# Performance work log

Hardware: AMD Instinct MI355X
Metric: run time of the kernel (lower is better)

## Reference

```python
import jax, jax.numpy as jnp
import numpy as np

N_HOST = 20000   # Host nodes
N_FLOW = 200000  # NetworkFlow nodes
E_HF = 400000    # edges per communicates direction
E_REL = 800000   # NetworkFlow-related-NetworkFlow edges
G = 64           # graphs in batch
H = 128          # hidden_dim
FI = 97          # NetworkFlow input feature dim (hardcoded in source)
NC = 10          # num_classes
L = 3            # layers
VOCAB = 4000     # host embedding table size (hardcoded in source)


def setup_inputs() -> dict:
    key = jax.random.key(0)
    ks = iter(jax.random.split(key, 40))
    def n(shape, scale=1.0):
        return jax.random.normal(next(ks), shape, jnp.float32) * scale
    s = 0.02
    inp = {}
    inp['host_node_ids'] = jax.random.randint(next(ks), (N_HOST,), 0, VOCAB)
    inp['flow_x'] = n((N_FLOW, FI))
    inp['h2f_src'] = jax.random.randint(next(ks), (E_HF,), 0, N_HOST)
    inp['h2f_dst'] = jax.random.randint(next(ks), (E_HF,), 0, N_FLOW)
    inp['f2h_src'] = jax.random.randint(next(ks), (E_HF,), 0, N_FLOW)
    inp['f2h_dst'] = jax.random.randint(next(ks), (E_HF,), 0, N_HOST)
    inp['rel_src'] = jax.random.randint(next(ks), (E_REL,), 0, N_FLOW)
    inp['rel_dst'] = jax.random.randint(next(ks), (E_REL,), 0, N_FLOW)
    inp['flow_batch'] = jnp.sort(jax.random.randint(next(ks), (N_FLOW,), 0, G))
    # parameters
    inp['host_embed'] = n((VOCAB, H), s)
    # layer 0 (heterogeneous input dims): GraphConv = lin_rel(agg) + lin_root(x_dst)
    inp['Wr0_h2f'] = n((H, H), s);  inp['br0_h2f'] = jnp.zeros((H,), jnp.float32); inp['Wo0_h2f'] = n((FI, H), s)
    inp['Wr0_f2h'] = n((FI, H), s); inp['br0_f2h'] = jnp.zeros((H,), jnp.float32); inp['Wo0_f2h'] = n((H, H), s)
    inp['Wr0_rel'] = n((FI, H), s); inp['br0_rel'] = jnp.zeros((H,), jnp.float32); inp['Wo0_rel'] = n((FI, H), s)
    # layers 1..L-1 stacked: axis1 order = [h2f, f2h, rel]
    inp['Wr'] = n((L - 1, 3, H, H), s)
    inp['br'] = jnp.zeros((L - 1, 3, H), jnp.float32)
    inp['Wo'] = n((L - 1, 3, H, H), s)
    # classifier (second Linear corrected to hidden//2 -> hidden so shapes chain)
    inp['Wc1'] = n((H, H // 2), s); inp['bc1'] = jnp.zeros((H // 2,), jnp.float32)
    inp['Wc2'] = n((H // 2, H), s); inp['bc2'] = jnp.zeros((H,), jnp.float32)
    inp['Wc3'] = n((H, NC), s);     inp['bc3'] = jnp.zeros((NC,), jnp.float32)
    return inp


def _graphconv(x_src, x_dst, src, dst, n_dst, Wr, br, Wo):
    # PyG GraphConv: lin_rel(sum_{j in N(i)} x_j) + lin_root(x_i); lin_root has no bias
    agg = jax.ops.segment_sum(x_src[src], dst, num_segments=n_dst)  # [n_dst, d_src]
    return agg @ Wr + br + x_dst @ Wo


def reference(host_node_ids, flow_x, h2f_src, h2f_dst, f2h_src, f2h_dst, rel_src, rel_dst,
              flow_batch, host_embed,
              Wr0_h2f, br0_h2f, Wo0_h2f, Wr0_f2h, br0_f2h, Wo0_f2h, Wr0_rel, br0_rel, Wo0_rel,
              Wr, br, Wo, Wc1, bc1, Wc2, bc2, Wc3, bc3):
    x_host = host_embed[host_node_ids]  # [N_HOST, H]
    x_flow = flow_x                     # [N_FLOW, FI]
    # layer 0: HeteroConv aggr='sum' over edge types writing to same dst type
    nf = _graphconv(x_host, x_flow, h2f_src, h2f_dst, N_FLOW, Wr0_h2f, br0_h2f, Wo0_h2f) \
       + _graphconv(x_flow, x_flow, rel_src, rel_dst, N_FLOW, Wr0_rel, br0_rel, Wo0_rel)
    nh = _graphconv(x_flow, x_host, f2h_src, f2h_dst, N_HOST, Wr0_f2h, br0_f2h, Wo0_f2h)
    x_flow, x_host = jax.nn.relu(nf), jax.nn.relu(nh)  # dropout p=0.0 -> identity
    # layers 1..L-1 (relu after all but the last conv)
    for l in range(L - 1):
        nf = _graphconv(x_host, x_flow, h2f_src, h2f_dst, N_FLOW, Wr[l, 0], br[l, 0], Wo[l, 0]) \
           + _graphconv(x_flow, x_flow, rel_src, rel_dst, N_FLOW, Wr[l, 2], br[l, 2], Wo[l, 2])
        nh = _graphconv(x_flow, x_host, f2h_src, f2h_dst, N_HOST, Wr[l, 1], br[l, 1], Wo[l, 1])
        if l < L - 2:
            nf, nh = jax.nn.relu(nf), jax.nn.relu(nh)
        x_flow, x_host = nf, nh
    pooled = jax.ops.segment_max(x_flow, flow_batch, num_segments=G)  # global_max_pool [G, H]
    h = jax.nn.relu(pooled @ Wc1 + bc1)
    h = jax.nn.relu(h @ Wc2 + bc2)
    return h @ Wc3 + bc3  # [G, NC]
```

## Files before the change

kernel.cpp:

```cpp
#include <hip/hip_runtime.h>
#include <hip/hip_bf16.h>

using bf16 = __hip_bfloat16;

#define N_HOSTN 20000
#define N_FLOWN 200000
#define E_HFN   400000
#define E_RELN  800000
#define E_CMBN  1200000
#define GG      64
#define HH      128
#define FIN     97
#define NCN     10

#define NB_REL_E 3125
#define NB_HF_E  1563
#define NB_CMB_N 782
#define NB_F2H_N 79
#define NCH_REL 391
#define NCH_HF  196
#define PLC_REL (NCH_REL*8)
#define PLC_H2F (PLC_REL + NCH_HF*8)
#define PLC_ALL (PLC_H2F + NCH_HF*8)

#define AGG_CAP    768
#define AGGF_DPW   24
#define AGGF_BLK   2084
#define AGGH_DPW   12
#define AGGH_BLK   417

static inline int cdiv(long long a, long long b){ return (int)((a + b - 1) / b); }

__device__ __forceinline__ float bf2f(unsigned short u){
    return __uint_as_float(((unsigned)u) << 16);
}
__device__ __forceinline__ unsigned short f2bf(float f){
    unsigned u = __float_as_uint(f);
    unsigned r = u + 0x7FFFu + ((u >> 16) & 1u);
    return (unsigned short)(r >> 16);
}
__device__ __forceinline__ float loadf(const void* p, size_t i, int isbf){
    return isbf ? bf2f(((const unsigned short*)p)[i]) : ((const float*)p)[i];
}
__device__ __forceinline__ void acc8(float* a, uint4 z){
    a[0] += __uint_as_float(z.x << 16);
    a[1] += __uint_as_float(z.x & 0xFFFF0000u);
    a[2] += __uint_as_float(z.y << 16);
    a[3] += __uint_as_float(z.y & 0xFFFF0000u);
    a[4] += __uint_as_float(z.z << 16);
    a[5] += __uint_as_float(z.z & 0xFFFF0000u);
    a[6] += __uint_as_float(z.w << 16);
    a[7] += __uint_as_float(z.w & 0xFFFF0000u);
}

__global__ void k_detect(const unsigned short* x, int* flag){
    __shared__ int bad;
    if (threadIdx.x == 0) bad = 0;
    __syncthreads();
    int b = 0;
    for (int i = threadIdx.x; i < 4096; i += 256) {
        unsigned e = (x[i] >> 7) & 0xFFu;
        if (e >= 0x90u) b++;
    }
    if (b) atomicAdd(&bad, b);
    __syncthreads();
    if (threadIdx.x == 0) *flag = (bad == 0) ? 1 : 0;
}

__global__ void k_zero(float* p, size_t n){
    size_t i = (size_t)blockIdx.x * 256 + threadIdx.x;
    if (i < n) p[i] = 0.f;
}
__global__ void k_flag_us(unsigned short* out, int n, unsigned short val){
    int i = blockIdx.x * 256 + threadIdx.x;
    if (i < n) out[i] = val;
}
__global__ void k_gather_embed(const int* ids, const void* emb, float* out, const int* flagp){
    int i = blockIdx.x * 256 + threadIdx.x;
    if (i >= N_HOSTN * HH) return;
    int isbf = *flagp;
    int node = i >> 7, f = i & 127;
    out[i] = loadf(emb, (size_t)ids[node] * HH + f, isbf);
}
__global__ void k_pad_cast(const void* x, unsigned short* o, const int* flagp){
    int i = blockIdx.x * 256 + threadIdx.x;
    if (i >= N_FLOWN * 16) return;
    int isbf = *flagp;
    int row = i >> 4, c0 = (i & 15) * 8;
    unsigned short v[8];
    #pragma unroll
    for (int j = 0; j < 8; ++j) {
        int c = c0 + j;
        v[j] = (c < FIN) ? f2bf(loadf(x, (size_t)row * FIN + c, isbf)) : (unsigned short)0;
    }
    uint4 ov;
    ov.x = (unsigned)v[0] | ((unsigned)v[1] << 16);
    ov.y = (unsigned)v[2] | ((unsigned)v[3] << 16);
    ov.z = (unsigned)v[4] | ((unsigned)v[5] << 16);
    ov.w = (unsigned)v[6] | ((unsigned)v[7] << 16);
    *(uint4*)(o + (size_t)row * 128 + c0) = ov;
}

__global__ __launch_bounds__(256) void k_wprep_all(
    const void* Wr0_h2f, const void* br0_h2f, const void* Wo0_h2f,
    const void* Wr0_f2h, const void* br0_f2h, const void* Wo0_f2h,
    const void* Wr0_rel, const void* br0_rel, const void* Wo0_rel,
    const void* Wr_all, const void* br_all, const void* Wo_all,
    unsigned short* WBT0, unsigned short* WBT1, unsigned short* WBT2,
    float* w_h2f0, float* w_h2f1, float* w_h2f2,
    float* w_f2h0, float* w_f2h1, float* w_of2h0, float* w_of2h1,
    float* b_comb0, float* b_comb1, float* b_comb2, float* b_f2h0, float* b_f2h1,
    const int* flagp)
{
    const int bb = blockIdx.x, t = threadIdx.x;
    const int isbf = *flagp;
    if (bb < 384) {
        int layer = bb >> 7;
        int i = ((bb & 127) << 8) + t;
        int nn = i >> 7, k = i & 127;
        float v = 0.f;
        if (layer == 0) {
            if (k < FIN) {
                if (nn < 128) v = loadf(Wo0_h2f, (size_t)k*128+nn, isbf) + loadf(Wo0_rel, (size_t)k*128+nn, isbf);
                else          v = loadf(Wr0_rel, (size_t)k*128+(nn-128), isbf);
            }
        } else {
            size_t oW = (size_t)((layer - 1) * 3) * 16384;
            if (nn < 128) v = loadf(Wo_all, oW + (size_t)k*128+nn, isbf)
                            + loadf(Wo_all, oW + 2*16384 + (size_t)k*128+nn, isbf);
            else          v = loadf(Wr_all, oW + 2*16384 + (size_t)k*128+(nn-128), isbf);
        }
        unsigned short* W = (layer == 0) ? WBT0 : ((layer == 1) ? WBT1 : WBT2);
        W[(size_t)nn*128 + k] = f2bf(v);
    } else if (bb < 576) {
        int r = bb - 384; int layer = r >> 6; int i = ((r & 63) << 8) + t;
        float v;
        if (layer == 0) v = loadf(Wr0_h2f, (size_t)i, isbf);
        else            v = loadf(Wr_all, (size_t)((layer-1)*3)*16384 + i, isbf);
        ((layer == 0) ? w_h2f0 : ((layer == 1) ? w_h2f1 : w_h2f2))[i] = v;
    } else if (bb < 640) {
        int i = ((bb - 576) << 8) + t;
        int k = i >> 7;
        w_f2h0[i] = (k < FIN) ? loadf(Wr0_f2h, (size_t)i, isbf) : 0.f;
    } else if (bb < 704) {
        int i = ((bb - 640) << 8) + t;
        w_f2h1[i] = loadf(Wr_all, (size_t)1*16384 + i, isbf);
    } else if (bb < 768) {
        int i = ((bb - 704) << 8) + t;
        w_of2h0[i] = loadf(Wo0_f2h, (size_t)i, isbf);
    } else if (bb < 832) {
        int i = ((bb - 768) << 8) + t;
        w_of2h1[i] = loadf(Wo_all, (size_t)1*16384 + i, isbf);
    } else {
        if (t < 128) {
            b_comb0[t] = loadf(br0_h2f, t, isbf) + loadf(br0_rel, t, isbf);
            b_comb1[t] = loadf(br_all, 0*128 + t, isbf) + loadf(br_all, 2*128 + t, isbf);
            b_comb2[t] = loadf(br_all, 3*128 + t, isbf) + loadf(br_all, 5*128 + t, isbf);
            b_f2h0[t]  = loadf(br0_f2h, t, isbf);
            b_f2h1[t]  = loadf(br_all, 1*128 + t, isbf);
        }
    }
}

__global__ void k_zero2(int* c0, int* c1){
    int bb = blockIdx.x, t = threadIdx.x;
    if (bb < NB_CMB_N) { int i = bb * 256 + t; if (i < N_FLOWN) c0[i] = 0; }
    else               { int i = (bb - NB_CMB_N) * 256 + t; if (i < N_HOSTN) c1[i] = 0; }
}
__global__ void k_hist3(const int* drel, const int* dh2f, const int* df2h,
                        int* c_cmb, int* c_f2h){
    int bb = blockIdx.x, t = threadIdx.x;
    const int* dst; int* cnt; int E; int base;
    if (bb < NB_REL_E)                   { dst = drel; cnt = c_cmb; E = E_RELN; base = bb; }
    else if (bb < NB_REL_E + NB_HF_E)    { dst = dh2f; cnt = c_cmb; E = E_HFN;  base = bb - NB_REL_E; }
    else                                 { dst = df2h; cnt = c_f2h; E = E_HFN;  base = bb - NB_REL_E - NB_HF_E; }
    int e = base * 256 + t;
    if (e < E) atomicAdd(&cnt[dst[e]], 1);
}
__global__ __launch_bounds__(256) void k_scan1_2(
    const int* c0, int* rp0, int* bs0,
    const int* c1, int* rp1, int* bs1)
{
    __shared__ int s[256];
    int bb = blockIdx.x, t = threadIdx.x;
    const int* cnt; int* rp; int* bsum; int n; int base;
    if (bb < NB_CMB_N) { cnt = c0; rp = rp0; bsum = bs0; n = N_FLOWN; base = bb; }
    else               { cnt = c1; rp = rp1; bsum = bs1; n = N_HOSTN; base = bb - NB_CMB_N; }
    int i = base * 256 + t;
    int v = (i < n) ? cnt[i] : 0;
    s[t] = v; __syncthreads();
    for (int off = 1; off < 256; off <<= 1) {
        int x = (t >= off) ? s[t - off] : 0;
        __syncthreads();
        s[t] += x;
        __syncthreads();
    }
    if (i < n) rp[i] = s[t] - v;
    if (t == 255) bsum[base] = s[255];
}
__global__ __launch_bounds__(256) void k_scan2_2(int* bs0, int* bs1){
    __shared__ int s[256];
    __shared__ int carry;
    int t = threadIdx.x;
    int* bsum; int nb;
    if (blockIdx.x == 0) { bsum = bs0; nb = NB_CMB_N; }
    else                 { bsum = bs1; nb = NB_F2H_N; }
    if (t == 0) carry = 0;
    __syncthreads();
    for (int base = 0; base < nb; base += 256) {
        int i = base + t;
        int v = (i < nb) ? bsum[i] : 0;
        s[t] = v; __syncthreads();
        for (int off = 1; off < 256; off <<= 1) {
            int x = (t >= off) ? s[t - off] : 0;
            __syncthreads();
            s[t] += x;
            __syncthreads();
        }
        int excl = s[t] - v + carry;
        if (i < nb) bsum[i] = excl;
        __syncthreads();
        if (t == 255) carry += s[255];
        __syncthreads();
    }
}
__global__ void k_scan3_2(int* rp0, const int* bs0, int* w0,
                          int* rp1, const int* bs1, int* w1)
{
    int bb = blockIdx.x, t = threadIdx.x;
    int* rp; const int* bsum; int* wr; int n, E, base;
    if (bb < NB_CMB_N) { rp = rp0; bsum = bs0; wr = w0; n = N_FLOWN; E = E_CMBN; base = bb; }
    else               { rp = rp1; bsum = bs1; wr = w1; n = N_HOSTN; E = E_HFN;  base = bb - NB_CMB_N; }
    int i = base * 256 + t;
    if (i < n) { int v = rp[i] + bsum[base]; rp[i] = v; wr[i] = v; }
    if (i == 0) rp[n] = E;
}
__global__ __launch_bounds__(256) void k_place3c(
    const int* s0, const int* d0,
    const int* s1, const int* d1,
    const int* s2, const int* d2,
    int* w_cmb, int* e_cmb, int* w_f2h, int* e_f2h)
{
    const int bb = blockIdx.x;
    const int *src, *dst; int *wr, *ei; int E, divc, rb, soff;
    if (bb < PLC_REL)      { src=s0; dst=d0; wr=w_cmb; ei=e_cmb; E=E_RELN; divc=25000; rb=bb;          soff=0; }
    else if (bb < PLC_H2F) { src=s1; dst=d1; wr=w_cmb; ei=e_cmb; E=E_HFN;  divc=25000; rb=bb-PLC_REL;  soff=N_FLOWN; }
    else                   { src=s2; dst=d2; wr=w_f2h; ei=e_f2h; E=E_HFN;  divc=2500;  rb=bb-PLC_H2F;  soff=0; }
    const int cls  = rb & 7;
    const int base = (rb >> 3) * 2048;
    const int t = threadIdx.x;
    #pragma unroll
    for (int i = 0; i < 8; ++i) {
        const int e = base + t + i * 256;
        if (e < E) {
            const int d = dst[e];
            if (d / divc == cls) {
                const int pos = atomicAdd(&wr[d], 1);
                ei[pos] = src[e] + soff;
            }
        }
    }
}

__global__ __launch_bounds__(256) void k_gemm128(
    const void* X, int xmode, const float* W, const float* bias,
    void* Y, int ybf, int M, int K, int accum, int dorelu, const int* flagp)
{
    const int isbf = (xmode == 2) ? *flagp : xmode;
    const int tid  = threadIdx.x;
    const int row0 = blockIdx.x * 16;
    __shared__ float sX[16][132];
    if (!isbf && (K & 3) == 0) {
        const int kq = K >> 2;
        for (int i = tid; i < 16 * kq; i += 256) {
            int r = i / kq, c4 = (i - r * kq) * 4;
            int gr = row0 + r;
            float4 v = {0.f, 0.f, 0.f, 0.f};
            if (gr < M) v = *(const float4*)((const float*)X + (size_t)gr * K + c4);
            *(float4*)&sX[r][c4] = v;
        }
    } else {
        const int total = 16 * K;
        for (int i = tid; i < total; i += 256) {
            int r = i / K, c = i - r * K;
            int gr = row0 + r;
            sX[r][c] = (gr < M) ? loadf(X, (size_t)gr * K + c, isbf) : 0.f;
        }
    }
    __syncthreads();

    const int c4 = (tid & 31) * 4;
    const int rb = tid >> 5;
    float a0x=0,a0y=0,a0z=0,a0w=0, a1x=0,a1y=0,a1z=0,a1w=0;
    #pragma unroll 4
    for (int k = 0; k < K; ++k) {
        const float4 w = *(const float4*)(W + (size_t)k * 128 + c4);
        const float x0 = sX[rb][k];
        const float x1 = sX[rb + 8][k];
        a0x = fmaf(x0, w.x, a0x); a0y = fmaf(x0, w.y, a0y);
        a0z = fmaf(x0, w.z, a0z); a0w = fmaf(x0, w.w, a0w);
        a1x = fmaf(x1, w.x, a1x); a1y = fmaf(x1, w.y, a1y);
        a1z = fmaf(x1, w.z, a1z); a1w = fmaf(x1, w.w, a1w);
    }
    float bx=0, by=0, bz=0, bw=0;
    if (bias) { const float4 b = *(const float4*)(bias + c4); bx=b.x; by=b.y; bz=b.z; bw=b.w; }

    #pragma unroll
    for (int h = 0; h < 2; ++h) {
        const int rr = row0 + rb + (h ? 8 : 0);
        if (rr >= M) continue;
        float v0 = (h?a1x:a0x)+bx, v1 = (h?a1y:a0y)+by;
        float v2 = (h?a1z:a0z)+bz, v3 = (h?a1w:a0w)+bw;
        if (ybf) {
            unsigned short* p = (unsigned short*)Y + (size_t)rr * 128 + c4;
            ushort4 o; o.x=f2bf(v0); o.y=f2bf(v1); o.z=f2bf(v2); o.w=f2bf(v3);
            *(ushort4*)p = o;
        } else {
            float* p = (float*)Y + (size_t)rr * 128 + c4;
            if (accum) { v0+=p[0]; v1+=p[1]; v2+=p[2]; v3+=p[3]; }
            if (dorelu) { v0=fmaxf(v0,0.f); v1=fmaxf(v1,0.f); v2=fmaxf(v2,0.f); v3=fmaxf(v3,0.f); }
            float4 o; o.x=v0; o.y=v1; o.z=v2; o.w=v3;
            *(float4*)p = o;
        }
    }
}

__global__ __launch_bounds__(256) void k_gemm2in(
    const float* __restrict__ X1, const float* __restrict__ X2,
    const float* __restrict__ W1, const float* __restrict__ W2,
    const float* __restrict__ bias, float* __restrict__ Y, int M)
{
    const int tid  = threadIdx.x;
    const int row0 = blockIdx.x * 16;
    __shared__ float sX1[16][132];
    __shared__ float sX2[16][132];
    for (int i = tid; i < 16 * 32; i += 256) {
        int r = i >> 5, c4 = (i & 31) * 4;
        int gr = row0 + r;
        float4 v1 = {0.f, 0.f, 0.f, 0.f}, v2 = {0.f, 0.f, 0.f, 0.f};
        if (gr < M) {
            v1 = *(const float4*)(X1 + (size_t)gr * 128 + c4);
            v2 = *(const float4*)(X2 + (size_t)gr * 128 + c4);
        }
        *(float4*)&sX1[r][c4] = v1;
        *(float4*)&sX2[r][c4] = v2;
    }
    __syncthreads();

    const int c4 = (tid & 31) * 4;
    const int rb = tid >> 5;
    float a0x=0,a0y=0,a0z=0,a0w=0, a1x=0,a1y=0,a1z=0,a1w=0;
    #pragma unroll 4
    for (int k = 0; k < 128; ++k) {
        const float4 w = *(const float4*)(W1 + (size_t)k * 128 + c4);
        const float x0 = sX1[rb][k];
        const float x1 = sX1[rb + 8][k];
        a0x = fmaf(x0, w.x, a0x); a0y = fmaf(x0, w.y, a0y);
        a0z = fmaf(x0, w.z, a0z); a0w = fmaf(x0, w.w, a0w);
        a1x = fmaf(x1, w.x, a1x); a1y = fmaf(x1, w.y, a1y);
        a1z = fmaf(x1, w.z, a1z); a1w = fmaf(x1, w.w, a1w);
    }
    #pragma unroll 4
    for (int k = 0; k < 128; ++k) {
        const float4 w = *(const float4*)(W2 + (size_t)k * 128 + c4);
        const float x0 = sX2[rb][k];
        const float x1 = sX2[rb + 8][k];
        a0x = fmaf(x0, w.x, a0x); a0y = fmaf(x0, w.y, a0y);
        a0z = fmaf(x0, w.z, a0z); a0w = fmaf(x0, w.w, a0w);
        a1x = fmaf(x1, w.x, a1x); a1y = fmaf(x1, w.y, a1y);
        a1z = fmaf(x1, w.z, a1z); a1w = fmaf(x1, w.w, a1w);
    }
    const float4 b = *(const float4*)(bias + c4);
    #pragma unroll
    for (int h = 0; h < 2; ++h) {
        const int rr = row0 + rb + (h ? 8 : 0);
        if (rr >= M) continue;
        float4 o;
        o.x = fmaxf((h?a1x:a0x) + b.x, 0.f);
        o.y = fmaxf((h?a1y:a0y) + b.y, 0.f);
        o.z = fmaxf((h?a1z:a0z) + b.z, 0.f);
        o.w = fmaxf((h?a1w:a0w) + b.w, 0.f);
        *(float4*)(Y + (size_t)rr * 128 + c4) = o;
    }
}

typedef __attribute__((ext_vector_type(8))) short bfrag;
typedef __attribute__((ext_vector_type(4))) float f32x4;

#define GEMM_CHUNKS 4
#define GEMM_MROWS  (32 * GEMM_CHUNKS)

__global__ __launch_bounds__(512, 4) void k_gemm_mfma(
    const unsigned short* __restrict__ Abf, const unsigned short* __restrict__ WBT,
    unsigned short* __restrict__ Y1, unsigned short* __restrict__ Y2, int M)
{
    __shared__ unsigned short sA[32 * 128];
    __shared__ unsigned short sO[2][32][136];

    const int tid  = threadIdx.x;
    const int wave = tid >> 6;
    const int lane = tid & 63;
    const int quad = lane >> 4;
    const int l16  = lane & 15;
    const int nbase = wave * 32;

    bfrag breg[4][2];
    #pragma unroll
    for (int c = 0; c < 4; ++c)
        #pragma unroll
        for (int j = 0; j < 2; ++j)
            breg[c][j] = *(const bfrag*)(WBT + (size_t)(nbase + j * 16 + l16) * 128
                                              + c * 32 + quad * 8);

// ... 198 lines not shown
            const int s2 = (e + 2 < Wcap) ? sIdx[wave][e + 2 - W0] : ei[e + 2];
            const int s3 = (e + 3 < Wcap) ? sIdx[wave][e + 3 - W0] : ei[e + 3];
            const uint4 z0 = *(const uint4*)(Z + (size_t)s0 * 128 + f8);
            const uint4 z1 = *(const uint4*)(Z + (size_t)s1 * 128 + f8);
            const uint4 z2 = *(const uint4*)(Z + (size_t)s2 * 128 + f8);
            const uint4 z3 = *(const uint4*)(Z + (size_t)s3 * 128 + f8);
            acc8(a, z0); acc8(a, z1); acc8(a, z2); acc8(a, z3);
            e += 4; n -= 4;
        }
        if (n & 2) {
            const int s0 = (e     < Wcap) ? sIdx[wave][e     - W0] : ei[e];
            const int s1 = (e + 1 < Wcap) ? sIdx[wave][e + 1 - W0] : ei[e + 1];
            const uint4 z0 = *(const uint4*)(Z + (size_t)s0 * 128 + f8);
            const uint4 z1 = *(const uint4*)(Z + (size_t)s1 * 128 + f8);
            acc8(a, z0); acc8(a, z1);
            e += 2;
        }
        if (n & 1) {
            const int s0 = (e < Wcap) ? sIdx[wave][e - W0] : ei[e];
            const uint4 z0 = *(const uint4*)(Z + (size_t)s0 * 128 + f8);
            acc8(a, z0);
        }

        if (act) {
            float4 oa, ob;
            oa.x = a[0]; oa.y = a[1]; oa.z = a[2]; oa.w = a[3];
            ob.x = a[4]; ob.y = a[5]; ob.z = a[6]; ob.w = a[7];
            *(float4*)(out + (size_t)d * 128 + f8)     = oa;
            *(float4*)(out + (size_t)d * 128 + f8 + 4) = ob;
        }
    }
}

#define PCHUNK 128
__global__ __launch_bounds__(128) void k_pool2(const unsigned short* xf, const int* batch,
                                               unsigned* bits){
    const int t = threadIdx.x;
    const int i0 = blockIdx.x * PCHUNK;
    const int iend = min(i0 + PCHUNK, N_FLOWN);
    if (i0 >= N_FLOWN) return;
    float cur = -3.4e38f;
    int curg = batch[i0];
    for (int i = i0; i < iend; ++i) {
        int g = batch[i];
        if (g != curg) {
            unsigned u = __float_as_uint(cur);
            unsigned ord = (u & 0x80000000u) ? ~u : (u | 0x80000000u);
            atomicMax(&bits[(size_t)curg * 128 + t], ord);
            cur = -3.4e38f; curg = g;
        }
        cur = fmaxf(cur, bf2f(xf[(size_t)i * 128 + t]));
    }
    unsigned u = __float_as_uint(cur);
    unsigned ord = (u & 0x80000000u) ? ~u : (u | 0x80000000u);
    atomicMax(&bits[(size_t)curg * 128 + t], ord);
}

__global__ __launch_bounds__(128) void k_classifier(
    const unsigned* bits,
    const void* Wc1, const void* bc1, const void* Wc2, const void* bc2,
    const void* Wc3, const void* bc3, void* out, const int* flagp)
{
    const int g = blockIdx.x, t = threadIdx.x;
    const int isbf = *flagp;
    __shared__ float sp[128], sh1[64], sh2[128];
    {
        unsigned ord = bits[(size_t)g * HH + t];
        unsigned u = (ord & 0x80000000u) ? (ord & 0x7FFFFFFFu) : ~ord;
        sp[t] = __uint_as_float(u);
    }
    __syncthreads();
    if (t < 64) {
        float a = loadf(bc1, t, isbf);
        #pragma unroll 4
        for (int k = 0; k < 128; ++k) a = fmaf(sp[k], loadf(Wc1, k * 64 + t, isbf), a);
        sh1[t] = fmaxf(a, 0.f);
    }
    __syncthreads();
    {
        float a = loadf(bc2, t, isbf);
        #pragma unroll 4
        for (int k = 0; k < 64; ++k) a = fmaf(sh1[k], loadf(Wc2, k * 128 + t, isbf), a);
        sh2[t] = fmaxf(a, 0.f);
    }
    __syncthreads();
    if (t < NCN) {
        float a = loadf(bc3, t, isbf);
        #pragma unroll 4
        for (int k = 0; k < 128; ++k) a = fmaf(sh2[k], loadf(Wc3, k * NCN + t, isbf), a);
        if (isbf) ((unsigned short*)out)[(size_t)g * NCN + t] = f2bf(a);
        else      ((float*)out)[(size_t)g * NCN + t] = a;
    }
}

extern "C" void kernel_launch(void* const* d_in, const int* in_sizes, int n_in,
                              void* d_out, int out_size, void* d_ws, size_t ws_size,
                              hipStream_t stream)
{
    const int*  host_ids   = (const int*) d_in[0];
    const void* flow_x     = d_in[1];
    const int*  h2f_src    = (const int*) d_in[2];
    const int*  h2f_dst    = (const int*) d_in[3];
    const int*  f2h_src    = (const int*) d_in[4];
    const int*  f2h_dst    = (const int*) d_in[5];
    const int*  rel_src    = (const int*) d_in[6];
    const int*  rel_dst    = (const int*) d_in[7];
    const int*  flow_batch = (const int*) d_in[8];
    const void* host_embed = d_in[9];
    const void* Wr0_h2f = d_in[10]; const void* br0_h2f = d_in[11]; const void* Wo0_h2f = d_in[12];
    const void* Wr0_f2h = d_in[13]; const void* br0_f2h = d_in[14]; const void* Wo0_f2h = d_in[15];
    const void* Wr0_rel = d_in[16]; const void* br0_rel = d_in[17]; const void* Wo0_rel = d_in[18];
    const void* Wr_all  = d_in[19];
    const void* br_all  = d_in[20];
    const void* Wo_all  = d_in[21];
    const void* Wc1 = d_in[22]; const void* bc1 = d_in[23];
    const void* Wc2 = d_in[24]; const void* bc2 = d_in[25];
    const void* Wc3 = d_in[26]; const void* bc3 = d_in[27];

    size_t off = 0;
    auto alloc = [&](size_t bytes) -> char* {
        char* p = (char*)d_ws + off;
        off += (bytes + 255) & ~(size_t)255;
        return p;
    };
    unsigned short* F1bf  = (unsigned short*)alloc((size_t)N_FLOWN * HH * 2);
    unsigned short* Froot = (unsigned short*)alloc((size_t)N_FLOWN * HH * 2);
    unsigned short* ZALL  = (unsigned short*)alloc((size_t)(N_FLOWN + N_HOSTN) * HH * 2);
    unsigned short* F2bf  = ZALL;
    unsigned short* HCbf  = ZALL + (size_t)N_FLOWN * HH;
    float* HA = (float*)alloc((size_t)N_HOSTN * HH * 4);
    float* HB = (float*)alloc((size_t)N_HOSTN * HH * 4);
    float* HD = (float*)alloc((size_t)N_HOSTN * HH * 4);
    unsigned short* WBT0 = (unsigned short*)alloc(256 * 128 * 2);
    unsigned short* WBT1 = (unsigned short*)alloc(256 * 128 * 2);
    unsigned short* WBT2 = (unsigned short*)alloc(256 * 128 * 2);
    float* w_h2f0  = (float*)alloc(128 * 128 * 4);
    float* w_h2f1  = (float*)alloc(128 * 128 * 4);
    float* w_h2f2  = (float*)alloc(128 * 128 * 4);
    float* w_f2h0  = (float*)alloc(128 * 128 * 4);
    float* w_f2h1  = (float*)alloc(128 * 128 * 4);
    float* w_of2h0 = (float*)alloc(128 * 128 * 4);
    float* w_of2h1 = (float*)alloc(128 * 128 * 4);
    float* b_comb0 = (float*)alloc(128 * 4);
    float* b_comb1 = (float*)alloc(128 * 4);
    float* b_comb2 = (float*)alloc(128 * 4);
    float* b_f2h0  = (float*)alloc(128 * 4);
    float* b_f2h1  = (float*)alloc(128 * 4);
    unsigned* poolbits = (unsigned*)alloc(GG * HH * 4);
    int* flagp = (int*)alloc(256);
    int* rp_cmb = (int*)alloc((N_FLOWN + 1) * 4);
    int* ei_cmb = (int*)alloc((size_t)E_CMBN * 4);
    int* rp_f2h = (int*)alloc((N_HOSTN + 1) * 4);
    int* ei_f2h = (int*)alloc((size_t)E_HFN * 4);
    int* wr_cmb = (int*)alloc((size_t)N_FLOWN * 4);
    int* wr_f2h = (int*)alloc((size_t)N_HOSTN * 4);
    int* bs0 = (int*)alloc(1024 * 4);
    int* bs2 = (int*)alloc(256 * 4);

    const int T = 256;
    #define GRID1(n) dim3(cdiv((long long)(n), T)), dim3(T), 0, stream

    if (off > ws_size) {
        k_flag_us<<<GRID1(out_size)>>>((unsigned short*)d_out, out_size, (unsigned short)0x4000);
        return;
    }

    k_detect<<<dim3(1), dim3(256), 0, stream>>>((const unsigned short*)flow_x, flagp);

    k_zero2 <<<dim3(NB_CMB_N + NB_F2H_N), dim3(256), 0, stream>>>(wr_cmb, wr_f2h);
    k_hist3 <<<dim3(NB_REL_E + 2*NB_HF_E), dim3(256), 0, stream>>>(rel_dst, h2f_dst, f2h_dst,
                                                                    wr_cmb, wr_f2h);
    k_scan1_2<<<dim3(NB_CMB_N + NB_F2H_N), dim3(256), 0, stream>>>(
        wr_cmb, rp_cmb, bs0, wr_f2h, rp_f2h, bs2);
    k_scan2_2<<<dim3(2), dim3(256), 0, stream>>>(bs0, bs2);
    k_scan3_2<<<dim3(NB_CMB_N + NB_F2H_N), dim3(256), 0, stream>>>(
        rp_cmb, bs0, wr_cmb, rp_f2h, bs2, wr_f2h);
    k_place3c<<<dim3(PLC_ALL), dim3(256), 0, stream>>>(
        rel_src, rel_dst, h2f_src, h2f_dst, f2h_src, f2h_dst,
        wr_cmb, ei_cmb, wr_f2h, ei_f2h);

    k_wprep_all<<<dim3(833), dim3(256), 0, stream>>>(
        Wr0_h2f, br0_h2f, Wo0_h2f, Wr0_f2h, br0_f2h, Wo0_f2h, Wr0_rel, br0_rel, Wo0_rel,
        Wr_all, br_all, Wo_all,
        WBT0, WBT1, WBT2, w_h2f0, w_h2f1, w_h2f2,
        w_f2h0, w_f2h1, w_of2h0, w_of2h1,
        b_comb0, b_comb1, b_comb2, b_f2h0, b_f2h1, flagp);

    k_gather_embed<<<GRID1(N_HOSTN * HH)>>>(host_ids, host_embed, HA, flagp);
    k_pad_cast<<<GRID1(N_FLOWN * 16)>>>(flow_x, F1bf, flagp);
    k_agg_host<<<dim3(AGGH_BLK), dim3(256), 0, stream>>>(F1bf, rp_f2h, ei_f2h, HD);
    k_gemm2in<<<dim3(cdiv(N_HOSTN,16)), dim3(256), 0, stream>>>(HD, HA, w_f2h0, w_of2h0, b_f2h0, HB, N_HOSTN);
    k_gemm128<<<dim3(cdiv(N_HOSTN,16)), dim3(256), 0, stream>>>(HA, 0, w_h2f0, nullptr, HCbf, 1, N_HOSTN, 128, 0, 0, flagp);
    k_gemm_mfma<<<dim3(cdiv(N_FLOWN, GEMM_MROWS)), dim3(512), 0, stream>>>(F1bf, WBT0, Froot, F2bf, N_FLOWN);
    k_agg_flow<<<dim3(AGGF_BLK), dim3(256), 0, stream>>>(ZALL, rp_cmb, ei_cmb,
                                                         Froot, b_comb0, F1bf, 1);

    k_agg_host<<<dim3(AGGH_BLK), dim3(256), 0, stream>>>(F1bf, rp_f2h, ei_f2h, HD);
    k_gemm128<<<dim3(cdiv(N_HOSTN,16)), dim3(256), 0, stream>>>(HB, 0, w_h2f1, nullptr, HCbf, 1, N_HOSTN, 128, 0, 0, flagp);
    k_gemm_mfma<<<dim3(cdiv(N_FLOWN, GEMM_MROWS)), dim3(512), 0, stream>>>(F1bf, WBT1, Froot, F2bf, N_FLOWN);
    k_agg_flow<<<dim3(AGGF_BLK), dim3(256), 0, stream>>>(ZALL, rp_cmb, ei_cmb,
                                                         Froot, b_comb1, F1bf, 1);
    k_gemm2in<<<dim3(cdiv(N_HOSTN,16)), dim3(256), 0, stream>>>(HD, HB, w_f2h1, w_of2h1, b_f2h1, HA, N_HOSTN);

    k_gemm128<<<dim3(cdiv(N_HOSTN,16)), dim3(256), 0, stream>>>(HA, 0, w_h2f2, nullptr, HCbf, 1, N_HOSTN, 128, 0, 0, flagp);
    k_gemm_mfma<<<dim3(cdiv(N_FLOWN, GEMM_MROWS)), dim3(512), 0, stream>>>(F1bf, WBT2, Froot, F2bf, N_FLOWN);
    k_agg_flow<<<dim3(AGGF_BLK), dim3(256), 0, stream>>>(ZALL, rp_cmb, ei_cmb,
                                                         Froot, b_comb2, F1bf, 0);

    k_zero<<<GRID1(GG * HH)>>>((float*)poolbits, (size_t)GG * HH);
    k_pool2<<<dim3(cdiv(N_FLOWN, PCHUNK)), dim3(128), 0, stream>>>(F1bf, flow_batch, poolbits);
    k_classifier<<<dim3(GG), dim3(128), 0, stream>>>(poolbits, Wc1, bc1, Wc2, bc2, Wc3, bc3,
                                                     d_out, flagp);
    #undef GRID1
}
```

Before: 941.4 us.

## Record per-edge ranks in histogram to make CSR placement atomic-free

The histogram kernel now stores the atomicAdd return value as each edge's rank within its destination bucket. The placement kernel then writes each edge directly to rowptr[dst] + rank, with no second round of atomics. This replaces the old 8-class partitioned scatter that re-read the edge arrays eight times. Rank and count scratch buffers reuse the HA/HB workspace, which assumes those buffers are free until they are written later. Ordering within a bucket becomes nondeterministic, but it already was.

```diff
diff --git a/kernel.cpp b/kernel.cpp
--- a/kernel.cpp
+++ b/kernel.cpp
@@ -17,11 +17,9 @@
 #define NB_HF_E  1563
 #define NB_CMB_N 782
 #define NB_F2H_N 79
-#define NCH_REL 391
-#define NCH_HF  196
-#define PLC_REL (NCH_REL*8)
-#define PLC_H2F (PLC_REL + NCH_HF*8)
-#define PLC_ALL (PLC_H2F + NCH_HF*8)
+#define PB_REL 782
+#define PB_HF  391
+#define PB_ALL (PB_REL + 2*PB_HF)
 
 #define AGG_CAP    768
 #define AGGF_DPW   24
@@ -168,14 +166,15 @@
     else               { int i = (bb - NB_CMB_N) * 256 + t; if (i < N_HOSTN) c1[i] = 0; }
 }
 __global__ void k_hist3(const int* drel, const int* dh2f, const int* df2h,
-                        int* c_cmb, int* c_f2h){
+                        int* c_cmb, int* c_f2h,
+                        int* rk_rel, int* rk_h2f, int* rk_f2h){
     int bb = blockIdx.x, t = threadIdx.x;
-    const int* dst; int* cnt; int E; int base;
-    if (bb < NB_REL_E)                   { dst = drel; cnt = c_cmb; E = E_RELN; base = bb; }
-    else if (bb < NB_REL_E + NB_HF_E)    { dst = dh2f; cnt = c_cmb; E = E_HFN;  base = bb - NB_REL_E; }
-    else                                 { dst = df2h; cnt = c_f2h; E = E_HFN;  base = bb - NB_REL_E - NB_HF_E; }
+    const int* dst; int* cnt; int* rk; int E; int base;
+    if (bb < NB_REL_E)                   { dst = drel; cnt = c_cmb; rk = rk_rel; E = E_RELN; base = bb; }
+    else if (bb < NB_REL_E + NB_HF_E)    { dst = dh2f; cnt = c_cmb; rk = rk_h2f; E = E_HFN;  base = bb - NB_REL_E; }
+    else                                 { dst = df2h; cnt = c_f2h; rk = rk_f2h; E = E_HFN;  base = bb - NB_REL_E - NB_HF_E; }
     int e = base * 256 + t;
-    if (e < E) atomicAdd(&cnt[dst[e]], 1);
+    if (e < E) rk[e] = atomicAdd(&cnt[dst[e]], 1);
 }
 __global__ __launch_bounds__(256) void k_scan1_2(
     const int* c0, int* rp0, int* bs0,
@@ -224,40 +223,36 @@
         __syncthreads();
     }
 }
-__global__ void k_scan3_2(int* rp0, const int* bs0, int* w0,
-                          int* rp1, const int* bs1, int* w1)
+__global__ void k_scan3_2(int* rp0, const int* bs0,
+                          int* rp1, const int* bs1)
 {
     int bb = blockIdx.x, t = threadIdx.x;
-    int* rp; const int* bsum; int* wr; int n, E, base;
-    if (bb < NB_CMB_N) { rp = rp0; bsum = bs0; wr = w0; n = N_FLOWN; E = E_CMBN; base = bb; }
-    else               { rp = rp1; bsum = bs1; wr = w1; n = N_HOSTN; E = E_HFN;  base = bb - NB_CMB_N; }
+    int* rp; const int* bsum; int n, E, base;
+    if (bb < NB_CMB_N) { rp = rp0; bsum = bs0; n = N_FLOWN; E = E_CMBN; base = bb; }
+    else               { rp = rp1; bsum = bs1; n = N_HOSTN; E = E_HFN;  base = bb - NB_CMB_N; }
     int i = base * 256 + t;
-    if (i < n) { int v = rp[i] + bsum[base]; rp[i] = v; wr[i] = v; }
+    if (i < n) rp[i] += bsum[base];
     if (i == 0) rp[n] = E;
 }
-__global__ __launch_bounds__(256) void k_place3c(
-    const int* s0, const int* d0,
-    const int* s1, const int* d1,
-    const int* s2, const int* d2,
-    int* w_cmb, int* e_cmb, int* w_f2h, int* e_f2h)
+__global__ __launch_bounds__(256) void k_place3(
+    const int* s0, const int* d0, const int* r0,
+    const int* s1, const int* d1, const int* r1,
+    const int* s2, const int* d2, const int* r2,
+    const int* rp_cmb, const int* rp_f2h,
+    int* e_cmb, int* e_f2h)
 {
     const int bb = blockIdx.x;
-    const int *src, *dst; int *wr, *ei; int E, divc, rb, soff;
-    if (bb < PLC_REL)      { src=s0; dst=d0; wr=w_cmb; ei=e_cmb; E=E_RELN; divc=25000; rb=bb;          soff=0; }
-    else if (bb < PLC_H2F) { src=s1; dst=d1; wr=w_cmb; ei=e_cmb; E=E_HFN;  divc=25000; rb=bb-PLC_REL;  soff=N_FLOWN; }
-    else                   { src=s2; dst=d2; wr=w_f2h; ei=e_f2h; E=E_HFN;  divc=2500;  rb=bb-PLC_H2F;  soff=0; }
-    const int cls  = rb & 7;
-    const int base = (rb >> 3) * 2048;
+    const int *src, *dst, *rank, *rp; int* ei; int E, base, soff;
+    if (bb < PB_REL)             { src=s0; dst=d0; rank=r0; rp=rp_cmb; ei=e_cmb; E=E_RELN; base=bb;               soff=0; }
+    else if (bb < PB_REL+PB_HF)  { src=s1; dst=d1; rank=r1; rp=rp_cmb; ei=e_cmb; E=E_HFN;  base=bb-PB_REL;        soff=N_FLOWN; }
+    else                         { src=s2; dst=d2; rank=r2; rp=rp_f2h; ei=e_f2h; E=E_HFN;  base=bb-PB_REL-PB_HF;  soff=0; }
     const int t = threadIdx.x;
     #pragma unroll
-    for (int i = 0; i < 8; ++i) {
-        const int e = base + t + i * 256;
+    for (int i = 0; i < 4; ++i) {
+        const int e = base * 1024 + i * 256 + t;
         if (e < E) {
             const int d = dst[e];
-            if (d / divc == cls) {
-                const int pos = atomicAdd(&wr[d], 1);
-                ei[pos] = src[e] + soff;
-            }
+            ei[rp[d] + rank[e]] = src[e] + soff;
         }
     }
 }
@@ -763,10 +758,13 @@
     int* ei_cmb = (int*)alloc((size_t)E_CMBN * 4);
     int* rp_f2h = (int*)alloc((N_HOSTN + 1) * 4);
     int* ei_f2h = (int*)alloc((size_t)E_HFN * 4);
-    int* wr_cmb = (int*)alloc((size_t)N_FLOWN * 4);
-    int* wr_f2h = (int*)alloc((size_t)N_HOSTN * 4);
     int* bs0 = (int*)alloc(1024 * 4);
     int* bs2 = (int*)alloc(256 * 4);
+    int* rk_rel = (int*)HA;
+    int* rk_h2f = rk_rel + E_RELN;
+    int* rk_f2h = rk_h2f + E_HFN;
+    int* c_cmb  = (int*)HB;
+    int* c_f2h  = c_cmb + N_FLOWN;
 
     const int T = 256;
     #define GRID1(n) dim3(cdiv((long long)(n), T)), dim3(T), 0, stream
@@ -778,17 +776,20 @@
 
     k_detect<<<dim3(1), dim3(256), 0, stream>>>((const unsigned short*)flow_x, flagp);
 
-    k_zero2 <<<dim3(NB_CMB_N + NB_F2H_N), dim3(256), 0, stream>>>(wr_cmb, wr_f2h);
+    k_zero2 <<<dim3(NB_CMB_N + NB_F2H_N), dim3(256), 0, stream>>>(c_cmb, c_f2h);
     k_hist3 <<<dim3(NB_REL_E + 2*NB_HF_E), dim3(256), 0, stream>>>(rel_dst, h2f_dst, f2h_dst,
-                                                                    wr_cmb, wr_f2h);
+                                                                    c_cmb, c_f2h,
+                                                                    rk_rel, rk_h2f, rk_f2h);
     k_scan1_2<<<dim3(NB_CMB_N + NB_F2H_N), dim3(256), 0, stream>>>(
-        wr_cmb, rp_cmb, bs0, wr_f2h, rp_f2h, bs2);
+        c_cmb, rp_cmb, bs0, c_f2h, rp_f2h, bs2);
     k_scan2_2<<<dim3(2), dim3(256), 0, stream>>>(bs0, bs2);
     k_scan3_2<<<dim3(NB_CMB_N + NB_F2H_N), dim3(256), 0, stream>>>(
-        rp_cmb, bs0, wr_cmb, rp_f2h, bs2, wr_f2h);
-    k_place3c<<<dim3(PLC_ALL), dim3(256), 0, stream>>>(
-        rel_src, rel_dst, h2f_src, h2f_dst, f2h_src, f2h_dst,
-        wr_cmb, ei_cmb, wr_f2h, ei_f2h);
+        rp_cmb, bs0, rp_f2h, bs2);
+    k_place3<<<dim3(PB_ALL), dim3(256), 0, stream>>>(
+        rel_src, rel_dst, rk_rel,
+        h2f_src, h2f_dst, rk_h2f,
+        f2h_src, f2h_dst, rk_f2h,
+        rp_cmb, rp_f2h, ei_cmb, ei_f2h);
 
     k_wprep_all<<<dim3(833), dim3(256), 0, stream>>>(
         Wr0_h2f, br0_h2f, Wo0_h2f, Wr0_f2h, br0_f2h, Wo0_f2h, Wr0_rel, br0_rel, Wo0_rel,
```

After: 914.4 us. -2.9%, faster.

## Build CSR via two-level binned counting sort with shared-memory atomics

Applied to the files above, without the earlier changes.

Replaces the global-atomic histogram, three-pass scan and class-partitioned placement with a two-level counting sort. Edges are first binned by destination>>8 using per-block shared-memory histograms and scattered into packed bin buffers that reuse the HA/HB scratch space. Each bin block then builds its local CSR row pointers and edge order with shared atomics. The aim is to cut global atomic contention and the repeated edge reads of the old 8-class placement, at the cost of an extra pass over packed edges and reliance on 18-bit source packing.

```diff
diff --git a/kernel.cpp b/kernel.cpp
--- a/kernel.cpp
+++ b/kernel.cpp
@@ -13,15 +13,13 @@
 #define FIN     97
 #define NCN     10
 
-#define NB_REL_E 3125
-#define NB_HF_E  1563
-#define NB_CMB_N 782
-#define NB_F2H_N 79
-#define NCH_REL 391
-#define NCH_HF  196
-#define PLC_REL (NCH_REL*8)
-#define PLC_H2F (PLC_REL + NCH_HF*8)
-#define PLC_ALL (PLC_H2F + NCH_HF*8)
+#define NBIN_F  782
+#define NBIN_H  79
+#define NBIN_ALL (NBIN_F + NBIN_H)
+#define BH_F    128
+#define BH_H    32
+#define EPB_F   9375
+#define EPB_H   12500
 
 #define AGG_CAP    768
 #define AGGF_DPW   24
@@ -162,54 +160,70 @@
     }
 }
 
-__global__ void k_zero2(int* c0, int* c1){
-    int bb = blockIdx.x, t = threadIdx.x;
-    if (bb < NB_CMB_N) { int i = bb * 256 + t; if (i < N_FLOWN) c0[i] = 0; }
-    else               { int i = (bb - NB_CMB_N) * 256 + t; if (i < N_HOSTN) c1[i] = 0; }
-}
-__global__ void k_hist3(const int* drel, const int* dh2f, const int* df2h,
-                        int* c_cmb, int* c_f2h){
-    int bb = blockIdx.x, t = threadIdx.x;
-    const int* dst; int* cnt; int E; int base;
-    if (bb < NB_REL_E)                   { dst = drel; cnt = c_cmb; E = E_RELN; base = bb; }
-    else if (bb < NB_REL_E + NB_HF_E)    { dst = dh2f; cnt = c_cmb; E = E_HFN;  base = bb - NB_REL_E; }
-    else                                 { dst = df2h; cnt = c_f2h; E = E_HFN;  base = bb - NB_REL_E - NB_HF_E; }
-    int e = base * 256 + t;
-    if (e < E) atomicAdd(&cnt[dst[e]], 1);
-}
-__global__ __launch_bounds__(256) void k_scan1_2(
-    const int* c0, int* rp0, int* bs0,
-    const int* c1, int* rp1, int* bs1)
-{
-    __shared__ int s[256];
-    int bb = blockIdx.x, t = threadIdx.x;
-    const int* cnt; int* rp; int* bsum; int n; int base;
-    if (bb < NB_CMB_N) { cnt = c0; rp = rp0; bsum = bs0; n = N_FLOWN; base = bb; }
-    else               { cnt = c1; rp = rp1; bsum = bs1; n = N_HOSTN; base = bb - NB_CMB_N; }
-    int i = base * 256 + t;
-    int v = (i < n) ? cnt[i] : 0;
+
+__global__ __launch_bounds__(256) void k_binhist(
+    const int* __restrict__ rel_dst, const int* __restrict__ h2f_dst,
+    const int* __restrict__ f2h_dst, int* __restrict__ cntF, int* __restrict__ cntH)
+{
+    __shared__ int c[NBIN_F];
+    const int t = threadIdx.x, bb = blockIdx.x;
+    if (bb < BH_F) {
+        for (int i = t; i < NBIN_F; i += 256) c[i] = 0;
+        __syncthreads();
+        const int e0 = bb * EPB_F;
+        for (int i = t; i < EPB_F; i += 256) {
+            const int e = e0 + i;
+            const int d = (e < E_RELN) ? rel_dst[e] : h2f_dst[e - E_RELN];
+            atomicAdd(&c[d >> 8], 1);
+        }
+        __syncthreads();
+        for (int i = t; i < NBIN_F; i += 256) cntF[i * BH_F + bb] = c[i];
+    } else {
+        const int blk = bb - BH_F;
+        for (int i = t; i < NBIN_H; i += 256) c[i] = 0;
+        __syncthreads();
+        const int e0 = blk * EPB_H;
+        for (int i = t; i < EPB_H; i += 256)
+            atomicAdd(&c[f2h_dst[e0 + i] >> 8], 1);
+        __syncthreads();
+        for (int i = t; i < NBIN_H; i += 256) cntH[i * BH_H + blk] = c[i];
+    }
+}
+__global__ __launch_bounds__(128) void k_binscan1(
+    int* __restrict__ cntF, int* __restrict__ cntH,
+    int* __restrict__ bintotF, int* __restrict__ bintotH)
+{
+    __shared__ int s[128];
+    const int t = threadIdx.x, b = blockIdx.x;
+    int v;
+    if (b < NBIN_F) v = (t < BH_F) ? cntF[b * BH_F + t] : 0;
+    else            v = (t < BH_H) ? cntH[(b - NBIN_F) * BH_H + t] : 0;
     s[t] = v; __syncthreads();
-    for (int off = 1; off < 256; off <<= 1) {
+    for (int off = 1; off < 128; off <<= 1) {
         int x = (t >= off) ? s[t - off] : 0;
         __syncthreads();
         s[t] += x;
         __syncthreads();
     }
-    if (i < n) rp[i] = s[t] - v;
-    if (t == 255) bsum[base] = s[255];
-}
-__global__ __launch_bounds__(256) void k_scan2_2(int* bs0, int* bs1){
+    if (b < NBIN_F) {
+        if (t < BH_F) cntF[b * BH_F + t] = s[t] - v;
+        if (t == 127) bintotF[b] = s[127];
+    } else {
+        if (t < BH_H) cntH[(b - NBIN_F) * BH_H + t] = s[t] - v;
+        if (t == 127) bintotH[b - NBIN_F] = s[127];
+    }
+}
+__global__ __launch_bounds__(256) void k_binscan2(int* aF, int* aH){
     __shared__ int s[256];
     __shared__ int carry;
-    int t = threadIdx.x;
-    int* bsum; int nb;
-    if (blockIdx.x == 0) { bsum = bs0; nb = NB_CMB_N; }
-    else                 { bsum = bs1; nb = NB_F2H_N; }
+    int* a; int n;
+    if (blockIdx.x == 0) { a = aF; n = NBIN_F; } else { a = aH; n = NBIN_H; }
+    const int t = threadIdx.x;
     if (t == 0) carry = 0;
     __syncthreads();
-    for (int base = 0; base < nb; base += 256) {
-        int i = base + t;
-        int v = (i < nb) ? bsum[i] : 0;
+    for (int base = 0; base < n; base += 256) {
+        const int i = base + t;
+        int v = (i < n) ? a[i] : 0;
         s[t] = v; __syncthreads();
         for (int off = 1; off < 256; off <<= 1) {
             int x = (t >= off) ? s[t - off] : 0;
@@ -218,47 +232,89 @@
             __syncthreads();
         }
         int excl = s[t] - v + carry;
-        if (i < nb) bsum[i] = excl;
+        if (i < n) a[i] = excl;
         __syncthreads();
         if (t == 255) carry += s[255];
         __syncthreads();
     }
 }
-__global__ void k_scan3_2(int* rp0, const int* bs0, int* w0,
-                          int* rp1, const int* bs1, int* w1)
-{
-    int bb = blockIdx.x, t = threadIdx.x;
-    int* rp; const int* bsum; int* wr; int n, E, base;
-    if (bb < NB_CMB_N) { rp = rp0; bsum = bs0; wr = w0; n = N_FLOWN; E = E_CMBN; base = bb; }
-    else               { rp = rp1; bsum = bs1; wr = w1; n = N_HOSTN; E = E_HFN;  base = bb - NB_CMB_N; }
-    int i = base * 256 + t;
-    if (i < n) { int v = rp[i] + bsum[base]; rp[i] = v; wr[i] = v; }
-    if (i == 0) rp[n] = E;
-}
-__global__ __launch_bounds__(256) void k_place3c(
-    const int* s0, const int* d0,
-    const int* s1, const int* d1,
-    const int* s2, const int* d2,
-    int* w_cmb, int* e_cmb, int* w_f2h, int* e_f2h)
-{
-    const int bb = blockIdx.x;
-    const int *src, *dst; int *wr, *ei; int E, divc, rb, soff;
-    if (bb < PLC_REL)      { src=s0; dst=d0; wr=w_cmb; ei=e_cmb; E=E_RELN; divc=25000; rb=bb;          soff=0; }
-    else if (bb < PLC_H2F) { src=s1; dst=d1; wr=w_cmb; ei=e_cmb; E=E_HFN;  divc=25000; rb=bb-PLC_REL;  soff=N_FLOWN; }
-    else                   { src=s2; dst=d2; wr=w_f2h; ei=e_f2h; E=E_HFN;  divc=2500;  rb=bb-PLC_H2F;  soff=0; }
-    const int cls  = rb & 7;
-    const int base = (rb >> 3) * 2048;
-    const int t = threadIdx.x;
-    #pragma unroll
-    for (int i = 0; i < 8; ++i) {
-        const int e = base + t + i * 256;
-        if (e < E) {
-            const int d = dst[e];
-            if (d / divc == cls) {
-                const int pos = atomicAdd(&wr[d], 1);
-                ei[pos] = src[e] + soff;
-            }
-        }
+__global__ __launch_bounds__(256) void k_binscatter(
+    const int* __restrict__ rel_src, const int* __restrict__ rel_dst,
+    const int* __restrict__ h2f_src, const int* __restrict__ h2f_dst,
+    const int* __restrict__ f2h_src, const int* __restrict__ f2h_dst,
+    const int* __restrict__ pbF, const int* __restrict__ pbH,
+    const int* __restrict__ bsF, const int* __restrict__ bsH,
+    unsigned* __restrict__ ebinF, unsigned* __restrict__ ebinH)
+{
+    __shared__ int base[NBIN_F];
+    const int t = threadIdx.x, bb = blockIdx.x;
+    if (bb < BH_F) {
+        for (int i = t; i < NBIN_F; i += 256) base[i] = bsF[i] + pbF[i * BH_F + bb];
+        __syncthreads();
+        const int e0 = bb * EPB_F;
+        for (int i = t; i < EPB_F; i += 256) {
+            const int e = e0 + i;
+            int d, sv;
+            if (e < E_RELN) { d = rel_dst[e]; sv = rel_src[e]; }
+            else            { d = h2f_dst[e - E_RELN]; sv = h2f_src[e - E_RELN] + N_FLOWN; }
+            const int pos = atomicAdd(&base[d >> 8], 1);
+            ebinF[pos] = (unsigned)sv | ((unsigned)(d & 255) << 18);
+        }
+    } else {
+        const int blk = bb - BH_F;
+        for (int i = t; i < NBIN_H; i += 256) base[i] = bsH[i] + pbH[i * BH_H + blk];
+        __syncthreads();
+        const int e0 = blk * EPB_H;
+        for (int i = t; i < EPB_H; i += 256) {
+            const int e = e0 + i;
+            const int d = f2h_dst[e];
+            const int pos = atomicAdd(&base[d >> 8], 1);
+            ebinH[pos] = (unsigned)f2h_src[e] | ((unsigned)(d & 255) << 18);
+        }
+    }
+}
+__global__ __launch_bounds__(256) void k_bincsr(
+    const unsigned* __restrict__ ebinF, const unsigned* __restrict__ ebinH,
+    const int* __restrict__ bsF, const int* __restrict__ bsH,
+    int* __restrict__ rp_cmb, int* __restrict__ ei_cmb,
+    int* __restrict__ rp_f2h, int* __restrict__ ei_f2h)
+{
+    __shared__ int c[256];
+    __shared__ int off[256];
+    const int t = threadIdx.x, b = blockIdx.x;
+    const unsigned* ebin; int* rp; int* ei; int seg0, seg1, dstbase, ndst;
+    if (b < NBIN_F) {
+        ebin = ebinF; rp = rp_cmb; ei = ei_cmb;
+        seg0 = bsF[b]; seg1 = (b == NBIN_F - 1) ? E_CMBN : bsF[b + 1];
+        dstbase = b * 256; ndst = min(256, N_FLOWN - dstbase);
+        if (b == 0 && t == 0) rp_cmb[N_FLOWN] = E_CMBN;
+    } else {
+        const int bh = b - NBIN_F;
+        ebin = ebinH; rp = rp_f2h; ei = ei_f2h;
+        seg0 = bsH[bh]; seg1 = (bh == NBIN_H - 1) ? E_HFN : bsH[bh + 1];
+        dstbase = bh * 256; ndst = min(256, N_HOSTN - dstbase);
+        if (bh == 0 && t == 0) rp_f2h[N_HOSTN] = E_HFN;
+    }
+    c[t] = 0;
+    __syncthreads();
+    for (int i = seg0 + t; i < seg1; i += 256)
+        atomicAdd(&c[ebin[i] >> 18], 1);
+    __syncthreads();
+    const int v = c[t];
+    for (int o = 1; o < 256; o <<= 1) {
+        int x = (t >= o) ? c[t - o] : 0;
+        __syncthreads();
+        c[t] += x;
+        __syncthreads();
+    }
+    const int excl = c[t] - v;
+    if (t < ndst) rp[dstbase + t] = seg0 + excl;
+    off[t] = seg0 + excl;
+    __syncthreads();
+    for (int i = seg0 + t; i < seg1; i += 256) {
+        const unsigned u = ebin[i];
+        const int pos = atomicAdd(&off[u >> 18], 1);
+        ei[pos] = (int)(u & 0x3FFFFu);
     }
 }
 
@@ -763,10 +819,12 @@
     int* ei_cmb = (int*)alloc((size_t)E_CMBN * 4);
     int* rp_f2h = (int*)alloc((N_HOSTN + 1) * 4);
     int* ei_f2h = (int*)alloc((size_t)E_HFN * 4);
-    int* wr_cmb = (int*)alloc((size_t)N_FLOWN * 4);
-    int* wr_f2h = (int*)alloc((size_t)N_HOSTN * 4);
-    int* bs0 = (int*)alloc(1024 * 4);
-    int* bs2 = (int*)alloc(256 * 4);
+    unsigned* ebinF = (unsigned*)HA;
+    unsigned* ebinH = ebinF + E_CMBN;
+    int* cntF    = (int*)HB;
+    int* cntH    = cntF + NBIN_F * BH_F;
+    int* bintotF = cntH + NBIN_H * BH_H;
+    int* bintotH = bintotF + NBIN_F;
 
     const int T = 256;
     #define GRID1(n) dim3(cdiv((long long)(n), T)), dim3(T), 0, stream
@@ -778,17 +836,14 @@
 
     k_detect<<<dim3(1), dim3(256), 0, stream>>>((const unsigned short*)flow_x, flagp);
 
-    k_zero2 <<<dim3(NB_CMB_N + NB_F2H_N), dim3(256), 0, stream>>>(wr_cmb, wr_f2h);
-    k_hist3 <<<dim3(NB_REL_E + 2*NB_HF_E), dim3(256), 0, stream>>>(rel_dst, h2f_dst, f2h_dst,
-                                                                    wr_cmb, wr_f2h);
-    k_scan1_2<<<dim3(NB_CMB_N + NB_F2H_N), dim3(256), 0, stream>>>(
-        wr_cmb, rp_cmb, bs0, wr_f2h, rp_f2h, bs2);
-    k_scan2_2<<<dim3(2), dim3(256), 0, stream>>>(bs0, bs2);
-    k_scan3_2<<<dim3(NB_CMB_N + NB_F2H_N), dim3(256), 0, stream>>>(
-        rp_cmb, bs0, wr_cmb, rp_f2h, bs2, wr_f2h);
-    k_place3c<<<dim3(PLC_ALL), dim3(256), 0, stream>>>(
+    k_binhist   <<<dim3(BH_F + BH_H), dim3(256), 0, stream>>>(rel_dst, h2f_dst, f2h_dst, cntF, cntH);
+    k_binscan1  <<<dim3(NBIN_ALL), dim3(128), 0, stream>>>(cntF, cntH, bintotF, bintotH);
+    k_binscan2  <<<dim3(2), dim3(256), 0, stream>>>(bintotF, bintotH);
+    k_binscatter<<<dim3(BH_F + BH_H), dim3(256), 0, stream>>>(
         rel_src, rel_dst, h2f_src, h2f_dst, f2h_src, f2h_dst,
-        wr_cmb, ei_cmb, wr_f2h, ei_f2h);
+        cntF, cntH, bintotF, bintotH, ebinF, ebinH);
+    k_bincsr    <<<dim3(NBIN_ALL), dim3(256), 0, stream>>>(
+        ebinF, ebinH, bintotF, bintotH, rp_cmb, ei_cmb, rp_f2h, ei_f2h);
 
     k_wprep_all<<<dim3(833), dim3(256), 0, stream>>>(
         Wr0_h2f, br0_h2f, Wo0_h2f, Wr0_f2h, br0_f2h, Wo0_f2h, Wr0_rel, br0_rel, Wo0_rel,
```

New measurement: 885.3 us. -6.0%, faster.
